# Kernel tuning notes

Hardware: AMD Instinct MI355X
Metric: run time of the kernel (lower is better)

The kernel has to match this reference:

```python
import jax, jax.numpy as jnp
import numpy as np

B = 16384
D_VIS, D_LANG, D_STATE = 768, 768, 64
D = 256          # d_model
E = 4            # n_experts
K = 2            # top_k
D_IN = D_VIS + D_LANG + D_STATE
EPS = 1e-5


def layernorm(x, g, b):
    mu = x.mean(-1, keepdims=True)
    var = ((x - mu) ** 2).mean(-1, keepdims=True)
    return g * (x - mu) / jnp.sqrt(var + EPS) + b


def setup_inputs() -> dict:
    key = jax.random.key(0)
    ks = jax.random.split(key, 16)
    s = 0.02
    return {
        "vis": jax.random.normal(ks[0], (B, D_VIS), jnp.float32),
        "lang": jax.random.normal(ks[1], (B, D_LANG), jnp.float32),
        "state": jax.random.normal(ks[2], (B, D_STATE), jnp.float32),
        # fusion: Linear(d_in, d_model) + LayerNorm
        "Wf": jax.random.normal(ks[3], (D_IN, D), jnp.float32) * s,
        "bf": jnp.zeros((D,), jnp.float32),
        "gf": jnp.ones((D,), jnp.float32),
        "bfln": jnp.zeros((D,), jnp.float32),
        # gate (bias=False); random instead of zeros so routing is nontrivial
        "Wg": jax.random.normal(ks[4], (D, E), jnp.float32) * s,
        # stacked experts: Linear(d,2d) -> GELU -> Linear(2d,d) -> GELU -> Linear(d,d), then LN(x + net(x))
        "W1": jax.random.normal(ks[5], (E, D, 2 * D), jnp.float32) * s,
        "b1": jnp.zeros((E, 2 * D), jnp.float32),
        "W2": jax.random.normal(ks[6], (E, 2 * D, D), jnp.float32) * s,
        "b2": jnp.zeros((E, D), jnp.float32),
        "W3": jax.random.normal(ks[7], (E, D, D), jnp.float32) * s,
        "b3": jnp.zeros((E, D), jnp.float32),
        "eg": jnp.ones((E, D), jnp.float32),
        "eb": jnp.zeros((E, D), jnp.float32),
    }


def reference(vis, lang, state, Wf, bf, gf, bfln, Wg, W1, b1, W2, b2, W3, b3, eg, eb):
    gelu = lambda t: jax.nn.gelu(t, approximate=False)
    # fusion: Linear -> LayerNorm -> GELU  (dropout is eval-mode identity)
    x = jnp.concatenate([vis, lang, state], axis=-1) @ Wf + bf   # [B, D]
    x = gelu(layernorm(x, gf, bfln))

    logits = x @ Wg                                              # [B, E]
    all_probs = jax.nn.softmax(logits, axis=-1)
    top_vals, top_idx = jax.lax.top_k(logits, K)                 # [B, K]
    top_w = jax.nn.softmax(top_vals, axis=-1)                    # [B, K]

    # all experts densely (E small); original computes same math per masked subset
    h = gelu(jnp.einsum('bd,edh->beh', x, W1) + b1)              # [B, E, 2D]
    h = gelu(jnp.einsum('beh,ehd->bed', h, W2) + b2)             # [B, E, D]
    h = jnp.einsum('bed,edf->bef', h, W3) + b3                   # [B, E, D]
    y = layernorm(x[:, None, :] + h, eg, eb)                     # [B, E, D]

    # gather selected experts and combine with top-k weights
    y_sel = jnp.take_along_axis(y, top_idx[:, :, None], axis=1)  # [B, K, D]
    out = jnp.einsum('bk,bkd->bd', top_w, y_sel)                 # [B, D]

    # load-balance loss: importance x load
    counts = jnp.zeros((E,), x.dtype).at[top_idx.reshape(-1)].add(1.0)
    f_i = counts / (B * K)
    lb_loss = E * jnp.sum(f_i * all_probs.mean(0))
    return out, lb_loss
```

## Files before the change

### kernel.cpp

```cpp
#include <hip/hip_runtime.h>
#include <math.h>


typedef unsigned short u16;
typedef unsigned int u32;
typedef __attribute__((ext_vector_type(8))) short bf16x8;
typedef __attribute__((ext_vector_type(4))) float f32x4;

__device__ __forceinline__ float bf2f(u16 u) {
    union { u32 i; float f; } v; v.i = ((u32)u) << 16; return v.f;
}
__device__ __forceinline__ u16 f2bf(float f) {
    union { float f; u32 i; } v; v.f = f;
    u32 x = v.i;
    return (u16)((x + 0x7fffu + ((x >> 16) & 1u)) >> 16);
}
__device__ __forceinline__ float gelu_exact(float v) {
    return 0.5f * v * (1.0f + erff(v * 0.70710678118654752f));
}

typedef __attribute__((address_space(1))) void GV;
typedef __attribute__((address_space(3))) void SV;
__device__ __forceinline__ void gldlds(const void* g, void* l) {
    __builtin_amdgcn_global_load_lds((GV*)g, (SV*)l, 16, 0, 0);
}

__device__ __forceinline__ u32 pk2(u32 f0, u32 f1) {
    return __builtin_amdgcn_perm(f1, f0, 0x07060302);
}

__device__ __forceinline__ void stageA64(const u16* Ag, int lda, u16* As, int tid) {
#pragma unroll
    for (int i = 0; i < 2; ++i) {
        int s = i * 256 + tid;
        int m = s >> 3, c = s & 7;
        gldlds(Ag + m * lda + (c ^ (m & 7)) * 8, As + s * 8);
    }
}
__device__ __forceinline__ void stageA64_R32(const u16* Ag, int lda, u16* As, int tid) {
    int s = tid;
    int m = s >> 3, c = s & 7;
    gldlds(Ag + m * lda + (c ^ (m & 7)) * 8, As + s * 8);
}
__device__ __forceinline__ void stageB64(const u16* Bg, int ldb, u16* Bs, int tid) {
#pragma unroll
    for (int i = 0; i < 8; ++i) {
        int s = i * 256 + tid;
        int n = s >> 3, c = s & 7;
        gldlds(Bg + n * ldb + (c ^ (n & 7)) * 8, Bs + s * 8);
    }
}
__device__ __forceinline__ void compute64(const u16* As, const u16* Bs, f32x4 acc[4][4],
                                          int w, int l16, int quad) {
#pragma unroll
    for (int ks = 0; ks < 2; ++ks) {
        bf16x8 a[4];
#pragma unroll
        for (int mt = 0; mt < 4; ++mt) {
            int m = mt * 16 + l16;
            a[mt] = *(const bf16x8*)(As + m * 64 + (((ks * 4 + quad) ^ (m & 7)) << 3));
        }
#pragma unroll
        for (int nt = 0; nt < 4; ++nt) {
            int n = w * 64 + nt * 16 + l16;
            bf16x8 b = *(const bf16x8*)(Bs + n * 64 + (((ks * 4 + quad) ^ (n & 7)) << 3));
#pragma unroll
            for (int mt = 0; mt < 4; ++mt)
                acc[mt][nt] = __builtin_amdgcn_mfma_f32_16x16x32_bf16(a[mt], b, acc[mt][nt], 0, 0, 0);
        }
    }
}
__device__ __forceinline__ void compute64_R32(const u16* As, const u16* Bs, f32x4 acc[2][4],
                                              int w, int l16, int quad) {
#pragma unroll
    for (int ks = 0; ks < 2; ++ks) {
        bf16x8 a[2];
#pragma unroll
        for (int mt = 0; mt < 2; ++mt) {
            int m = mt * 16 + l16;
            a[mt] = *(const bf16x8*)(As + m * 64 + (((ks * 4 + quad) ^ (m & 7)) << 3));
        }
#pragma unroll
        for (int nt = 0; nt < 4; ++nt) {
            int n = w * 64 + nt * 16 + l16;
            bf16x8 b = *(const bf16x8*)(Bs + n * 64 + (((ks * 4 + quad) ^ (n & 7)) << 3));
#pragma unroll
            for (int mt = 0; mt < 2; ++mt)
                acc[mt][nt] = __builtin_amdgcn_mfma_f32_16x16x32_bf16(a[mt], b, acc[mt][nt], 0, 0, 0);
        }
    }
}

#define SEG_WF  409600
#define SEG_W1  524288
#define SEG_W2  524288
#define SEG_W3  262144
#define PREP_ITEMS (SEG_WF + SEG_W1 + SEG_W2 + SEG_W3 + 8)

__global__ __launch_bounds__(256) void prep_kernel(
    const float* __restrict__ Wf, const float* __restrict__ W1, const float* __restrict__ W2,
    const float* __restrict__ W3,
    u16* __restrict__ wft, u16* __restrict__ w1t, u16* __restrict__ w2t, u16* __restrict__ w3t,
    float* __restrict__ lbacc) {
    int idx = blockIdx.x * 256 + threadIdx.x;
    if (idx < SEG_WF) {
        int n = idx / 1600, k = idx % 1600;
        wft[idx] = f2bf(Wf[(size_t)k * 256 + n]);
        return;
    }
    idx -= SEG_WF;
    if (idx < SEG_W1) {
        int e = idx >> 17, r = idx & 131071;
        int n = r >> 8, k = r & 255;
        w1t[idx] = f2bf(W1[(size_t)e * 131072 + (size_t)k * 512 + n]);
        return;
    }
    idx -= SEG_W1;
    if (idx < SEG_W2) {
        int e = idx >> 17, r = idx & 131071;
        int n = r >> 9, k = r & 511;
        w2t[idx] = f2bf(W2[(size_t)e * 131072 + (size_t)k * 256 + n]);
        return;
    }
    idx -= SEG_W2;
    if (idx < SEG_W3) {
        int e = idx >> 16, r = idx & 65535;
        int n = r >> 8, k = r & 255;
        w3t[idx] = f2bf(W3[(size_t)e * 65536 + (size_t)k * 256 + n]);
        return;
    }
    idx -= SEG_W3;
    if (idx < 8) lbacc[idx] = 0.0f;
}

__global__ __launch_bounds__(256) void fusion_kernel(
    const float* __restrict__ vis, const float* __restrict__ lang, const float* __restrict__ state,
    const u16* __restrict__ BT, const float* __restrict__ bfv_, const float* __restrict__ gf,
    const float* __restrict__ bfln, const float* __restrict__ Wg,
    u16* __restrict__ xbf, float* __restrict__ wr, float* __restrict__ lbacc) {
    __shared__ __align__(16) u32 Af[2048];
    __shared__ __align__(16) u16 Bs[16384];
    int tid = threadIdx.x;
    int w = tid >> 6, lane = tid & 63, quad = lane >> 4, l16 = lane & 15;
    int m0 = blockIdx.x * 32;
    f32x4 acc[2][4] = {};

    for (int kit = 0; kit < 25; ++kit) {
        const float* base; int ld;
        if (kit < 12)      { base = vis   + (size_t)m0 * 768 + kit * 64;        ld = 768; }
        else if (kit < 24) { base = lang  + (size_t)m0 * 768 + (kit - 12) * 64; ld = 768; }
        else               { base = state + (size_t)m0 * 64;                    ld = 64; }
#pragma unroll
        for (int i = 0; i < 2; ++i) {
            int s = i * 256 + tid;
            int m = s >> 4, c = s & 15;
            gldlds(base + m * ld + (c ^ (m & 15)) * 4, Af + s * 4);
        }
        stageB64(BT + kit * 64, 1600, Bs, tid);
        __syncthreads();
#pragma unroll
        for (int ks = 0; ks < 2; ++ks) {
            bf16x8 a[2];
#pragma unroll
            for (int mt = 0; mt < 2; ++mt) {
                int m = mt * 16 + l16;
                int c0 = ks * 8 + quad * 2;
                const u32* rowp = Af + m * 64;
                uint4 f0 = *(const uint4*)(rowp + (c0 ^ (m & 15)) * 4);
                uint4 f1 = *(const uint4*)(rowp + ((c0 + 1) ^ (m & 15)) * 4);
                union { u32 u[4]; bf16x8 v; } pk;
                pk.u[0] = pk2(f0.x, f0.y); pk.u[1] = pk2(f0.z, f0.w);
                pk.u[2] = pk2(f1.x, f1.y); pk.u[3] = pk2(f1.z, f1.w);
                a[mt] = pk.v;
            }
#pragma unroll
            for (int nt = 0; nt < 4; ++nt) {
                int n = w * 64 + nt * 16 + l16;
                bf16x8 b = *(const bf16x8*)(Bs + n * 64 + (((ks * 4 + quad) ^ (n & 7)) << 3));
#pragma unroll
                for (int mt = 0; mt < 2; ++mt)
                    acc[mt][nt] = __builtin_amdgcn_mfma_f32_16x16x32_bf16(a[mt], b, acc[mt][nt], 0, 0, 0);
            }
        }
        __syncthreads();
    }

    float2* red  = (float2*)Af;
    float*  muv  = (float*)(Af + 256);
    float*  rsv  = (float*)(Af + 288);
    float*  gred = (float*)(Af + 512);
    float*  sacc = (float*)(Af + 1024);

    float bv[4], gvv[4], blv[4]; float4 wgv[4];
#pragma unroll
    for (int nt = 0; nt < 4; ++nt) {
        int col = w * 64 + nt * 16 + l16;
        bv[nt] = bfv_[col]; gvv[nt] = gf[col]; blv[nt] = bfln[col];
        wgv[nt] = *(const float4*)(Wg + col * 4);
    }
    if (tid < 8) sacc[tid] = 0.f;
#pragma unroll
    for (int mt = 0; mt < 2; ++mt)
#pragma unroll
        for (int r = 0; r < 4; ++r) {
            float ss = 0.f, qq = 0.f;
#pragma unroll
            for (int nt = 0; nt < 4; ++nt) {
                float v = acc[mt][nt][r] + bv[nt];
                acc[mt][nt][r] = v;
                ss += v; qq += v * v;
            }
#pragma unroll
            for (int d = 1; d < 16; d <<= 1) { ss += __shfl_xor(ss, d); qq += __shfl_xor(qq, d); }
            if (l16 == 0) red[w * 32 + mt * 16 + quad * 4 + r] = make_float2(ss, qq);
        }
    __syncthreads();
    if (tid < 32) {
        float ss = 0.f, qq = 0.f;
#pragma unroll
        for (int ww = 0; ww < 4; ++ww) { float2 t = red[ww * 32 + tid]; ss += t.x; qq += t.y; }
        float mu = ss * (1.f / 256.f);
        float var = qq * (1.f / 256.f) - mu * mu;
        muv[tid] = mu;
        rsv[tid] = 1.f / sqrtf(var + 1e-5f);
    }
    __syncthreads();
#pragma unroll
    for (int mt = 0; mt < 2; ++mt)
#pragma unroll
        for (int r = 0; r < 4; ++r) {
            int rl = mt * 16 + quad * 4 + r;
            float mu = muv[rl], rs = rsv[rl];
#pragma unroll
            for (int nt = 0; nt < 4; ++nt) {
                int col = w * 64 + nt * 16 + l16;
                float t = (acc[mt][nt][r] - mu) * rs * gvv[nt] + blv[nt];
                float g = gelu_exact(t);
                acc[mt][nt][r] = g;
                xbf[(size_t)(m0 + rl) * 256 + col] = f2bf(g);
            }
        }
#pragma unroll
    for (int mt = 0; mt < 2; ++mt)
#pragma unroll
        for (int r = 0; r < 4; ++r) {
            int rl = mt * 16 + quad * 4 + r;
            float p0 = 0.f, p1 = 0.f, p2 = 0.f, p3 = 0.f;
#pragma unroll
            for (int nt = 0; nt < 4; ++nt) {
                float g = acc[mt][nt][r];
                p0 += g * wgv[nt].x; p1 += g * wgv[nt].y;
                p2 += g * wgv[nt].z; p3 += g * wgv[nt].w;
            }
#pragma unroll
            for (int d = 1; d < 16; d <<= 1) {
                p0 += __shfl_xor(p0, d); p1 += __shfl_xor(p1, d);
                p2 += __shfl_xor(p2, d); p3 += __shfl_xor(p3, d);
            }
            if (l16 == 0) {
                float* gp = gred + w * 128 + rl * 4;
                gp[0] = p0; gp[1] = p1; gp[2] = p2; gp[3] = p3;
            }
        }
    __syncthreads();
    if (tid < 32) {
        int row = tid;
        float lg[4];
#pragma unroll
        for (int e = 0; e < 4; ++e)
            lg[e] = gred[row * 4 + e] + gred[128 + row * 4 + e] +
                    gred[256 + row * 4 + e] + gred[384 + row * 4 + e];
        float mx = fmaxf(fmaxf(lg[0], lg[1]), fmaxf(lg[2], lg[3]));
        float ex[4]; float Z = 0.f;
#pragma unroll
        for (int e = 0; e < 4; ++e) { ex[e] = expf(lg[e] - mx); Z += ex[e]; }
        int i0 = 0; float v0 = lg[0];
#pragma unroll
        for (int e = 1; e < 4; ++e) if (lg[e] > v0) { v0 = lg[e]; i0 = e; }
        int i1 = -1; float v1 = -1e30f;
#pragma unroll
        for (int e = 0; e < 4; ++e) if (e != i0 && lg[e] > v1) { v1 = lg[e]; i1 = e; }
        float t = expf(v1 - v0);
        float wA = 1.f / (1.f + t), wB = t / (1.f + t);
        float w4[4] = {0.f, 0.f, 0.f, 0.f};
        w4[i0] = wA; w4[i1] = wB;
#pragma unroll
        for (int e = 0; e < 4; ++e) wr[(size_t)(m0 + row) * 4 + e] = w4[e];
#pragma unroll
        for (int e = 0; e < 4; ++e) atomicAdd(&sacc[e], ex[e] / Z);
        atomicAdd(&sacc[4 + i0], 1.f);
        atomicAdd(&sacc[4 + i1], 1.f);
    }
    __syncthreads();
    if (tid < 8) atomicAdd(lbacc + tid, sacc[tid]);
}

__global__ __launch_bounds__(256) void expert_gemm_kernel(
    const u16* __restrict__ A, int lda, size_t aE,
    const u16* __restrict__ BT, size_t bE,
    const float* __restrict__ bias, int biasE,
    u16* __restrict__ outp, int ldo, size_t oE) {
    __shared__ __align__(16) u16 As[4096];
    __shared__ __align__(16) u16 Bs[16384];
    int tid = threadIdx.x;
    int w = tid >> 6, lane = tid & 63, quad = lane >> 4, l16 = lane & 15;
    int m0 = blockIdx.x * 64;
    int col0 = blockIdx.y * 256;
    int e = blockIdx.z;
    f32x4 acc[4][4] = {};
    const u16* Ag = A + e * aE + (size_t)m0 * lda;
    const u16* Bg = BT + e * bE + (size_t)col0 * lda;
    int kiters = lda >> 6;
    for (int kit = 0; kit < kiters; ++kit) {
        stageA64(Ag + kit * 64, lda, As, tid);
        stageB64(Bg + kit * 64, lda, Bs, tid);
        __syncthreads();
        compute64(As, Bs, acc, w, l16, quad);
        __syncthreads();
    }
#pragma unroll
    for (int nt = 0; nt < 4; ++nt) {
        int col = col0 + w * 64 + nt * 16 + l16;
        float bvv = bias[e * biasE + col];
#pragma unroll
        for (int mt = 0; mt < 4; ++mt)
#pragma unroll
            for (int r = 0; r < 4; ++r) {
                int row = m0 + mt * 16 + quad * 4 + r;
                outp[e * oE + (size_t)row * ldo + col] = f2bf(gelu_exact(acc[mt][nt][r] + bvv));
            }
    }
}

__global__ __launch_bounds__(256) void combine_kernel(
    const u16* __restrict__ h2, const u16* __restrict__ W3T,
    const float* __restrict__ b3, const float* __restrict__ eg, const float* __restrict__ eb,
    const u16* __restrict__ xbf, const float* __restrict__ wr,
    const float* __restrict__ lbacc, float* __restrict__ outp) {
    __shared__ __align__(16) u16 As[2048];
    __shared__ __align__(16) u16 Bs[16384];
    __shared__ __align__(16) u16 xs[8192];
    __shared__ float wl[128];
    int tid = threadIdx.x;
    int w = tid >> 6, lane = tid & 63, quad = lane >> 4, l16 = lane & 15;
    int m0 = blockIdx.x * 32;
    if (blockIdx.x == 0 && tid == 0) {
        float lb = 0.f;
#pragma unroll
        for (int e = 0; e < 4; ++e)
            lb += (lbacc[4 + e] / 32768.f) * (lbacc[e] / 16384.f);
        outp[4194304] = 4.f * lb;
    }
#pragma unroll
    for (int i = 0; i < 4; ++i) {
        int s = i * 256 + tid;
        *(uint4*)(xs + s * 8) = *(const uint4*)(xbf + (size_t)m0 * 256 + s * 8);
    }
    if (tid < 128) wl[tid] = wr[(size_t)m0 * 4 + tid];
    float2* red = (float2*)As;
    float* muv = (float*)((char*)As + 1024);
    float* rsv = (float*)((char*)As + 1152);
    f32x4 oacc[2][4] = {};
    for (int e = 0; e < 4; ++e) {
        __syncthreads();
        f32x4 acc[2][4] = {};
        const u16* Ag = h2 + ((size_t)e * 16384 + m0) * 256;
        const u16* Bg = W3T + (size_t)e * 65536;
        for (int kit = 0; kit < 4; ++kit) {
            stageA64_R32(Ag + kit * 64, 256, As, tid);
            stageB64(Bg + kit * 64, 256, Bs, tid);
            __syncthreads();
            compute64_R32(As, Bs, acc, w, l16, quad);
            __syncthreads();
        }
        float b3v[4], egv[4], ebv[4];
#pragma unroll
        for (int nt = 0; nt < 4; ++nt) {
            int col = w * 64 + nt * 16 + l16;
            b3v[nt] = b3[e * 256 + col]; egv[nt] = eg[e * 256 + col]; ebv[nt] = eb[e * 256 + col];
        }
#pragma unroll
        for (int mt = 0; mt < 2; ++mt)
#pragma unroll
            for (int r = 0; r < 4; ++r) {
                int rl = mt * 16 + quad * 4 + r;
                float ss = 0.f, qq = 0.f;
#pragma unroll
                for (int nt = 0; nt < 4; ++nt) {
                    int col = w * 64 + nt * 16 + l16;
                    float v = acc[mt][nt][r] + b3v[nt] + bf2f(xs[rl * 256 + col]);
                    acc[mt][nt][r] = v;
                    ss += v; qq += v * v;
                }
#pragma unroll
                for (int d = 1; d < 16; d <<= 1) { ss += __shfl_xor(ss, d); qq += __shfl_xor(qq, d); }
                if (l16 == 0) red[w * 32 + rl] = make_float2(ss, qq);
            }
        __syncthreads();
        if (tid < 32) {
            float ss = 0.f, qq = 0.f;
#pragma unroll
            for (int ww = 0; ww < 4; ++ww) { float2 t = red[ww * 32 + tid]; ss += t.x; qq += t.y; }
            float mu = ss * (1.f / 256.f);
            float var = qq * (1.f / 256.f) - mu * mu;
            muv[tid] = mu;
            rsv[tid] = 1.f / sqrtf(var + 1e-5f);
        }
        __syncthreads();
#pragma unroll
        for (int mt = 0; mt < 2; ++mt)
#pragma unroll
            for (int r = 0; r < 4; ++r) {
                int rl = mt * 16 + quad * 4 + r;
                float mu = muv[rl], rs = rsv[rl], we = wl[rl * 4 + e];
#pragma unroll
                for (int nt = 0; nt < 4; ++nt) {
                    float y = (acc[mt][nt][r] - mu) * rs * egv[nt] + ebv[nt];
                    oacc[mt][nt][r] += we * y;
                }
            }
    }
#pragma unroll
    for (int mt = 0; mt < 2; ++mt)
#pragma unroll
        for (int r = 0; r < 4; ++r) {
            int rl = mt * 16 + quad * 4 + r;
#pragma unroll
            for (int nt = 0; nt < 4; ++nt) {
                int col = w * 64 + nt * 16 + l16;
                outp[(size_t)(m0 + rl) * 256 + col] = oacc[mt][nt][r];
            }
        }
}

extern "C" void kernel_launch(void* const* d_in, const int* in_sizes, int n_in,
                              void* d_out, int out_size, void* d_ws, size_t ws_size,
                              hipStream_t stream) {
    const float* vis   = (const float*)d_in[0];
    const float* lang  = (const float*)d_in[1];
    const float* state = (const float*)d_in[2];
    const float* Wf    = (const float*)d_in[3];
    const float* bf_   = (const float*)d_in[4];
    const float* gf    = (const float*)d_in[5];
    const float* bfln  = (const float*)d_in[6];
    const float* Wg    = (const float*)d_in[7];
    const float* W1    = (const float*)d_in[8];
    const float* b1    = (const float*)d_in[9];
    const float* W2    = (const float*)d_in[10];
    const float* b2    = (const float*)d_in[11];
    const float* W3    = (const float*)d_in[12];
    const float* b3    = (const float*)d_in[13];
    const float* eg    = (const float*)d_in[14];
    const float* eb    = (const float*)d_in[15];
    float* outp = (float*)d_out;

    char* ws = (char*)d_ws;
    size_t off = 0;
    float* lbacc = (float*)(ws + off); off += 256;
    u16* WFT  = (u16*)(ws + off); off += 819200UL;
    u16* W1T  = (u16*)(ws + off); off += 1048576UL;
    u16* W2T  = (u16*)(ws + off); off += 1048576UL;
    u16* W3T  = (u16*)(ws + off); off += 524288UL;
    u16* XBF  = (u16*)(ws + off); off += 8388608UL;
    float* WR = (float*)(ws + off); off += 262144UL;
    u16* H1   = (u16*)(ws + off); off += 67108864UL;
    u16* H2   = (u16*)(ws + off); off += 33554432UL;
    if (ws_size < off) return;

    int prep_blocks = (PREP_ITEMS + 255) / 256;
    prep_kernel<<<prep_blocks, 256, 0, stream>>>(Wf, W1, W2, W3, WFT, W1T, W2T, W3T, lbacc);
    fusion_kernel<<<512, 256, 0, stream>>>(vis, lang, state, WFT, bf_, gf, bfln, Wg,
                                           XBF, WR, lbacc);
    expert_gemm_kernel<<<dim3(256, 2, 4), 256, 0, stream>>>(
        XBF, 256, 0, W1T, 131072, b1, 512, H1, 512, 8388608UL);
    expert_gemm_kernel<<<dim3(256, 1, 4), 256, 0, stream>>>(
        H1, 512, 8388608UL, W2T, 131072, b2, 256, H2, 256, 4194304UL);
    combine_kernel<<<512, 256, 0, stream>>>(H2, W3T, b3, eg, eb, XBF, WR, lbacc, outp);
}
```

Before: 324.5 us.

## Double-buffer LDS staging in fusion, expert and combine GEMM kernels

Turns the GEMM loops in all three kernels into double-buffered pipelines. The next K-tile is loaded asynchronously via global_load_lds while the current one is computed, using explicit vmcnt waits and raw barriers in place of __syncthreads. The combine kernel also flattens its expert and K loops into one 16-step pipeline, and moves the residual x tile into registers so it can reuse LDS. This is meant to hide global load latency. The cost is doubled LDS, which may reduce occupancy, and the hand-counted vmcnt values must match the number of issued loads.

```diff
diff --git a/kernel.cpp b/kernel.cpp
--- a/kernel.cpp
+++ b/kernel.cpp
@@ -28,6 +28,20 @@
 __device__ __forceinline__ u32 pk2(u32 f0, u32 f1) {
     return __builtin_amdgcn_perm(f1, f0, 0x07060302);
 }
+
+#define WAIT_VM(N) asm volatile("s_waitcnt vmcnt(" #N ")" ::: "memory")
+#define BARRIER()                                    \
+    do {                                             \
+        asm volatile("" ::: "memory");               \
+        __builtin_amdgcn_s_barrier();                \
+        asm volatile("" ::: "memory");               \
+    } while (0)
+#define LGKBAR()                                            \
+    do {                                                    \
+        asm volatile("s_waitcnt lgkmcnt(0)" ::: "memory");  \
+        __builtin_amdgcn_s_barrier();                       \
+        asm volatile("" ::: "memory");                      \
+    } while (0)
 
 __device__ __forceinline__ void stageA64(const u16* Ag, int lda, u16* As, int tid) {
 #pragma unroll
@@ -138,14 +152,14 @@
     const u16* __restrict__ BT, const float* __restrict__ bfv_, const float* __restrict__ gf,
     const float* __restrict__ bfln, const float* __restrict__ Wg,
     u16* __restrict__ xbf, float* __restrict__ wr, float* __restrict__ lbacc) {
-    __shared__ __align__(16) u32 Af[2048];
-    __shared__ __align__(16) u16 Bs[16384];
+    __shared__ __align__(16) u32 Af[2][2048];
+    __shared__ __align__(16) u16 Bs[2][16384];
     int tid = threadIdx.x;
     int w = tid >> 6, lane = tid & 63, quad = lane >> 4, l16 = lane & 15;
     int m0 = blockIdx.x * 32;
     f32x4 acc[2][4] = {};
 
-    for (int kit = 0; kit < 25; ++kit) {
+    auto stage = [&](int b, int kit) {
         const float* base; int ld;
         if (kit < 12)      { base = vis   + (size_t)m0 * 768 + kit * 64;        ld = 768; }
         else if (kit < 24) { base = lang  + (size_t)m0 * 768 + (kit - 12) * 64; ld = 768; }
@@ -154,10 +168,17 @@
         for (int i = 0; i < 2; ++i) {
             int s = i * 256 + tid;
             int m = s >> 4, c = s & 15;
-            gldlds(base + m * ld + (c ^ (m & 15)) * 4, Af + s * 4);
-        }
-        stageB64(BT + kit * 64, 1600, Bs, tid);
-        __syncthreads();
+            gldlds(base + m * ld + (c ^ (m & 15)) * 4, &Af[b][s * 4]);
+        }
+        stageB64(BT + kit * 64, 1600, Bs[b], tid);
+    };
+
+    stage(0, 0);
+    for (int kit = 0; kit < 25; ++kit) {
+        int cur = kit & 1;
+        if (kit + 1 < 25) { stage(cur ^ 1, kit + 1); WAIT_VM(10); }
+        else              { WAIT_VM(0); }
+        BARRIER();
 #pragma unroll
         for (int ks = 0; ks < 2; ++ks) {
             bf16x8 a[2];
@@ -165,7 +186,7 @@
             for (int mt = 0; mt < 2; ++mt) {
                 int m = mt * 16 + l16;
                 int c0 = ks * 8 + quad * 2;
-                const u32* rowp = Af + m * 64;
+                const u32* rowp = &Af[cur][m * 64];
                 uint4 f0 = *(const uint4*)(rowp + (c0 ^ (m & 15)) * 4);
                 uint4 f1 = *(const uint4*)(rowp + ((c0 + 1) ^ (m & 15)) * 4);
                 union { u32 u[4]; bf16x8 v; } pk;
@@ -176,20 +197,21 @@
 #pragma unroll
             for (int nt = 0; nt < 4; ++nt) {
                 int n = w * 64 + nt * 16 + l16;
-                bf16x8 b = *(const bf16x8*)(Bs + n * 64 + (((ks * 4 + quad) ^ (n & 7)) << 3));
+                bf16x8 b = *(const bf16x8*)(Bs[cur] + n * 64 + (((ks * 4 + quad) ^ (n & 7)) << 3));
 #pragma unroll
                 for (int mt = 0; mt < 2; ++mt)
                     acc[mt][nt] = __builtin_amdgcn_mfma_f32_16x16x32_bf16(a[mt], b, acc[mt][nt], 0, 0, 0);
             }
         }
-        __syncthreads();
-    }
-
-    float2* red  = (float2*)Af;
-    float*  muv  = (float*)(Af + 256);
-    float*  rsv  = (float*)(Af + 288);
-    float*  gred = (float*)(Af + 512);
-    float*  sacc = (float*)(Af + 1024);
+        BARRIER();
+    }
+
+    u32* Af0 = &Af[0][0];
+    float2* red  = (float2*)Af0;
+    float*  muv  = (float*)(Af0 + 256);
+    float*  rsv  = (float*)(Af0 + 288);
+    float*  gred = (float*)(Af0 + 512);
+    float*  sacc = (float*)(Af0 + 1024);
 
     float bv[4], gvv[4], blv[4]; float4 wgv[4];
 #pragma unroll
@@ -300,8 +322,8 @@
     const u16* __restrict__ BT, size_t bE,
     const float* __restrict__ bias, int biasE,
     u16* __restrict__ outp, int ldo, size_t oE) {
-    __shared__ __align__(16) u16 As[4096];
-    __shared__ __align__(16) u16 Bs[16384];
+    __shared__ __align__(16) u16 As[2][4096];
+    __shared__ __align__(16) u16 Bs[2][16384];
     int tid = threadIdx.x;
     int w = tid >> 6, lane = tid & 63, quad = lane >> 4, l16 = lane & 15;
     int m0 = blockIdx.x * 64;
@@ -311,12 +333,18 @@
     const u16* Ag = A + e * aE + (size_t)m0 * lda;
     const u16* Bg = BT + e * bE + (size_t)col0 * lda;
     int kiters = lda >> 6;
+    stageA64(Ag, lda, As[0], tid);
+    stageB64(Bg, lda, Bs[0], tid);
     for (int kit = 0; kit < kiters; ++kit) {
-        stageA64(Ag + kit * 64, lda, As, tid);
-        stageB64(Bg + kit * 64, lda, Bs, tid);
-        __syncthreads();
-        compute64(As, Bs, acc, w, l16, quad);
-        __syncthreads();
+        int cur = kit & 1;
+        if (kit + 1 < kiters) {
+            stageA64(Ag + (kit + 1) * 64, lda, As[cur ^ 1], tid);
+            stageB64(Bg + (kit + 1) * 64, lda, Bs[cur ^ 1], tid);
+            WAIT_VM(10);
+        } else { WAIT_VM(0); }
+        BARRIER();
+        compute64(As[cur], Bs[cur], acc, w, l16, quad);
+        BARRIER();
     }
 #pragma unroll
     for (int nt = 0; nt < 4; ++nt) {
@@ -337,10 +365,11 @@
     const float* __restrict__ b3, const float* __restrict__ eg, const float* __restrict__ eb,
     const u16* __restrict__ xbf, const float* __restrict__ wr,
     const float* __restrict__ lbacc, float* __restrict__ outp) {
-    __shared__ __align__(16) u16 As[2048];
-    __shared__ __align__(16) u16 Bs[16384];
-    __shared__ __align__(16) u16 xs[8192];
+    __shared__ __align__(16) u16 As[2][2048];
+    __shared__ __align__(16) u16 Bs[2][16384];
     __shared__ float wl[128];
+    __shared__ float2 red[128];
+    __shared__ float muv[32], rsv[32];
     int tid = threadIdx.x;
     int w = tid >> 6, lane = tid & 63, quad = lane >> 4, l16 = lane & 15;
     int m0 = blockIdx.x * 32;
@@ -351,74 +380,92 @@
             lb += (lbacc[4 + e] / 32768.f) * (lbacc[e] / 16384.f);
         outp[4194304] = 4.f * lb;
     }
+    u16* xs = &Bs[0][0];
 #pragma unroll
     for (int i = 0; i < 4; ++i) {
         int s = i * 256 + tid;
         *(uint4*)(xs + s * 8) = *(const uint4*)(xbf + (size_t)m0 * 256 + s * 8);
     }
     if (tid < 128) wl[tid] = wr[(size_t)m0 * 4 + tid];
-    float2* red = (float2*)As;
-    float* muv = (float*)((char*)As + 1024);
-    float* rsv = (float*)((char*)As + 1152);
+    __syncthreads();
+    float xr[2][4][4];
+#pragma unroll
+    for (int mt = 0; mt < 2; ++mt)
+#pragma unroll
+        for (int r = 0; r < 4; ++r) {
+            int rl = mt * 16 + quad * 4 + r;
+#pragma unroll
+            for (int nt = 0; nt < 4; ++nt) {
+                int col = w * 64 + nt * 16 + l16;
+                xr[mt][r][nt] = bf2f(xs[rl * 256 + col]);
+            }
+        }
+    __syncthreads();
+
     f32x4 oacc[2][4] = {};
-    for (int e = 0; e < 4; ++e) {
-        __syncthreads();
-        f32x4 acc[2][4] = {};
-        const u16* Ag = h2 + ((size_t)e * 16384 + m0) * 256;
-        const u16* Bg = W3T + (size_t)e * 65536;
-        for (int kit = 0; kit < 4; ++kit) {
-            stageA64_R32(Ag + kit * 64, 256, As, tid);
-            stageB64(Bg + kit * 64, 256, Bs, tid);
-            __syncthreads();
-            compute64_R32(As, Bs, acc, w, l16, quad);
-            __syncthreads();
-        }
-        float b3v[4], egv[4], ebv[4];
-#pragma unroll
-        for (int nt = 0; nt < 4; ++nt) {
-            int col = w * 64 + nt * 16 + l16;
-            b3v[nt] = b3[e * 256 + col]; egv[nt] = eg[e * 256 + col]; ebv[nt] = eb[e * 256 + col];
-        }
-#pragma unroll
-        for (int mt = 0; mt < 2; ++mt)
-#pragma unroll
-            for (int r = 0; r < 4; ++r) {
-                int rl = mt * 16 + quad * 4 + r;
+    f32x4 acc[2][4] = {};
+    auto stage = [&](int b, int p) {
+        int ee = p >> 2, kit = p & 3;
+        stageA64_R32(h2 + ((size_t)ee * 16384 + m0) * 256 + kit * 64, 256, As[b], tid);
+        stageB64(W3T + (size_t)ee * 65536 + kit * 64, 256, Bs[b], tid);
+    };
+    stage(0, 0);
+    for (int p = 0; p < 16; ++p) {
+        int cur = p & 1;
+        if (p + 1 < 16) { stage(cur ^ 1, p + 1); WAIT_VM(9); }
+        else            { WAIT_VM(0); }
+        BARRIER();
+        compute64_R32(As[cur], Bs[cur], acc, w, l16, quad);
+        BARRIER();
+        if ((p & 3) == 3) {
+            int e = p >> 2;
+            float b3v[4], egv[4], ebv[4];
+#pragma unroll
+            for (int nt = 0; nt < 4; ++nt) {
+                int col = w * 64 + nt * 16 + l16;
+                b3v[nt] = b3[e * 256 + col]; egv[nt] = eg[e * 256 + col]; ebv[nt] = eb[e * 256 + col];
+            }
+#pragma unroll
+            for (int mt = 0; mt < 2; ++mt)
+#pragma unroll
+                for (int r = 0; r < 4; ++r) {
+                    int rl = mt * 16 + quad * 4 + r;
+                    float ss = 0.f, qq = 0.f;
+#pragma unroll
+                    for (int nt = 0; nt < 4; ++nt) {
+                        float v = acc[mt][nt][r] + b3v[nt] + xr[mt][r][nt];
+                        acc[mt][nt][r] = v;
+                        ss += v; qq += v * v;
+                    }
+#pragma unroll
+                    for (int d = 1; d < 16; d <<= 1) { ss += __shfl_xor(ss, d); qq += __shfl_xor(qq, d); }
+                    if (l16 == 0) red[w * 32 + rl] = make_float2(ss, qq);
+                }
+            LGKBAR();
+            if (tid < 32) {
                 float ss = 0.f, qq = 0.f;
 #pragma unroll
-                for (int nt = 0; nt < 4; ++nt) {
-                    int col = w * 64 + nt * 16 + l16;
-                    float v = acc[mt][nt][r] + b3v[nt] + bf2f(xs[rl * 256 + col]);
-                    acc[mt][nt][r] = v;
-                    ss += v; qq += v * v;
+                for (int ww = 0; ww < 4; ++ww) { float2 t = red[ww * 32 + tid]; ss += t.x; qq += t.y; }
+                float mu = ss * (1.f / 256.f);
+                float var = qq * (1.f / 256.f) - mu * mu;
+                muv[tid] = mu;
+                rsv[tid] = 1.f / sqrtf(var + 1e-5f);
+            }
+            LGKBAR();
+#pragma unroll
+            for (int mt = 0; mt < 2; ++mt)
+#pragma unroll
+                for (int r = 0; r < 4; ++r) {
+                    int rl = mt * 16 + quad * 4 + r;
+                    float mu = muv[rl], rs = rsv[rl], we = wl[rl * 4 + e];
+#pragma unroll
+                    for (int nt = 0; nt < 4; ++nt) {
+                        float y = (acc[mt][nt][r] - mu) * rs * egv[nt] + ebv[nt];
+                        oacc[mt][nt][r] += we * y;
+                        acc[mt][nt][r] = 0.f;
+                    }
                 }
-#pragma unroll
-                for (int d = 1; d < 16; d <<= 1) { ss += __shfl_xor(ss, d); qq += __shfl_xor(qq, d); }
-                if (l16 == 0) red[w * 32 + rl] = make_float2(ss, qq);
-            }
-        __syncthreads();
-        if (tid < 32) {
-            float ss = 0.f, qq = 0.f;
-#pragma unroll
-            for (int ww = 0; ww < 4; ++ww) { float2 t = red[ww * 32 + tid]; ss += t.x; qq += t.y; }
-            float mu = ss * (1.f / 256.f);
-            float var = qq * (1.f / 256.f) - mu * mu;
-            muv[tid] = mu;
-            rsv[tid] = 1.f / sqrtf(var + 1e-5f);
-        }
-        __syncthreads();
-#pragma unroll
-        for (int mt = 0; mt < 2; ++mt)
-#pragma unroll
-            for (int r = 0; r < 4; ++r) {
-                int rl = mt * 16 + quad * 4 + r;
-                float mu = muv[rl], rs = rsv[rl], we = wl[rl * 4 + e];
-#pragma unroll
-                for (int nt = 0; nt < 4; ++nt) {
-                    float y = (acc[mt][nt][r] - mu) * rs * egv[nt] + ebv[nt];
-                    oacc[mt][nt][r] += we * y;
-                }
-            }
+        }
     }
 #pragma unroll
     for (int mt = 0; mt < 2; ++mt)
```

Measured after the change: 355.8 us. 1.1x slower.

## Double-buffer LDS staging in fusion, expert GEMM and combine kernels

Applied to the files above, without the earlier changes.

Adds ping-pong LDS buffers to all three GEMM kernels so the loads for the next K-slice are issued before computing the current one, leaving one barrier per step. The combine kernel now also runs a single 16-step pipeline across experts and K, calls the LN epilogue every four steps, and holds the residual x in registers instead of a separate LDS array. This is meant to hide global-load latency behind MFMA work. In exchange LDS use roughly doubles, which can lower occupancy, and register pressure rises from the cached residual.

```diff
diff --git a/kernel.cpp b/kernel.cpp
--- a/kernel.cpp
+++ b/kernel.cpp
@@ -138,14 +138,16 @@
     const u16* __restrict__ BT, const float* __restrict__ bfv_, const float* __restrict__ gf,
     const float* __restrict__ bfln, const float* __restrict__ Wg,
     u16* __restrict__ xbf, float* __restrict__ wr, float* __restrict__ lbacc) {
-    __shared__ __align__(16) u32 Af[2048];
-    __shared__ __align__(16) u16 Bs[16384];
+    __shared__ __align__(16) u32 AfA[2048];
+    __shared__ __align__(16) u32 AfB[2048];
+    __shared__ __align__(16) u16 BsA[16384];
+    __shared__ __align__(16) u16 BsB[16384];
     int tid = threadIdx.x;
     int w = tid >> 6, lane = tid & 63, quad = lane >> 4, l16 = lane & 15;
     int m0 = blockIdx.x * 32;
     f32x4 acc[2][4] = {};
 
-    for (int kit = 0; kit < 25; ++kit) {
+    auto stageK = [&](u32* Af, u16* Bs, int kit) {
         const float* base; int ld;
         if (kit < 12)      { base = vis   + (size_t)m0 * 768 + kit * 64;        ld = 768; }
         else if (kit < 24) { base = lang  + (size_t)m0 * 768 + (kit - 12) * 64; ld = 768; }
@@ -157,7 +159,8 @@
             gldlds(base + m * ld + (c ^ (m & 15)) * 4, Af + s * 4);
         }
         stageB64(BT + kit * 64, 1600, Bs, tid);
-        __syncthreads();
+    };
+    auto computeK = [&](const u32* Af, const u16* Bs) {
 #pragma unroll
         for (int ks = 0; ks < 2; ++ks) {
             bf16x8 a[2];
@@ -182,14 +185,27 @@
                     acc[mt][nt] = __builtin_amdgcn_mfma_f32_16x16x32_bf16(a[mt], b, acc[mt][nt], 0, 0, 0);
             }
         }
-        __syncthreads();
-    }
-
-    float2* red  = (float2*)Af;
-    float*  muv  = (float*)(Af + 256);
-    float*  rsv  = (float*)(Af + 288);
-    float*  gred = (float*)(Af + 512);
-    float*  sacc = (float*)(Af + 1024);
+    };
+
+    stageK(AfA, BsA, 0);
+    __syncthreads();
+    for (int kit = 0; kit < 24; kit += 2) {
+        stageK(AfB, BsB, kit + 1);
+        computeK(AfA, BsA);
+        __syncthreads();
+        if (kit + 2 < 25) stageK(AfA, BsA, kit + 2);
+        computeK(AfB, BsB);
+        __syncthreads();
+    }
+    computeK(AfA, BsA);
+    __syncthreads();
+
+    u32* Af0 = AfA;
+    float2* red  = (float2*)Af0;
+    float*  muv  = (float*)(Af0 + 256);
+    float*  rsv  = (float*)(Af0 + 288);
+    float*  gred = (float*)(Af0 + 512);
+    float*  sacc = (float*)(Af0 + 1024);
 
     float bv[4], gvv[4], blv[4]; float4 wgv[4];
 #pragma unroll
@@ -300,8 +316,10 @@
     const u16* __restrict__ BT, size_t bE,
     const float* __restrict__ bias, int biasE,
     u16* __restrict__ outp, int ldo, size_t oE) {
-    __shared__ __align__(16) u16 As[4096];
-    __shared__ __align__(16) u16 Bs[16384];
+    __shared__ __align__(16) u16 AsA[4096];
+    __shared__ __align__(16) u16 AsB[4096];
+    __shared__ __align__(16) u16 BsA[16384];
+    __shared__ __align__(16) u16 BsB[16384];
     int tid = threadIdx.x;
     int w = tid >> 6, lane = tid & 63, quad = lane >> 4, l16 = lane & 15;
     int m0 = blockIdx.x * 64;
@@ -311,11 +329,19 @@
     const u16* Ag = A + e * aE + (size_t)m0 * lda;
     const u16* Bg = BT + e * bE + (size_t)col0 * lda;
     int kiters = lda >> 6;
-    for (int kit = 0; kit < kiters; ++kit) {
-        stageA64(Ag + kit * 64, lda, As, tid);
-        stageB64(Bg + kit * 64, lda, Bs, tid);
-        __syncthreads();
-        compute64(As, Bs, acc, w, l16, quad);
+    stageA64(Ag, lda, AsA, tid);
+    stageB64(Bg, lda, BsA, tid);
+    __syncthreads();
+    for (int kit = 0; kit < kiters; kit += 2) {
+        stageA64(Ag + (kit + 1) * 64, lda, AsB, tid);
+        stageB64(Bg + (kit + 1) * 64, lda, BsB, tid);
+        compute64(AsA, BsA, acc, w, l16, quad);
+        __syncthreads();
+        if (kit + 2 < kiters) {
+            stageA64(Ag + (kit + 2) * 64, lda, AsA, tid);
+            stageB64(Bg + (kit + 2) * 64, lda, BsA, tid);
+        }
+        compute64(AsB, BsB, acc, w, l16, quad);
         __syncthreads();
     }
 #pragma unroll
@@ -337,10 +363,13 @@
     const float* __restrict__ b3, const float* __restrict__ eg, const float* __restrict__ eb,
     const u16* __restrict__ xbf, const float* __restrict__ wr,
     const float* __restrict__ lbacc, float* __restrict__ outp) {
-    __shared__ __align__(16) u16 As[2048];
-    __shared__ __align__(16) u16 Bs[16384];
-    __shared__ __align__(16) u16 xs[8192];
+    __shared__ __align__(16) u16 AsA[2048];
+    __shared__ __align__(16) u16 AsB[2048];
+    __shared__ __align__(16) u16 BsA[16384];
+    __shared__ __align__(16) u16 BsB[16384];
     __shared__ float wl[128];
+    __shared__ float2 red[128];
+    __shared__ float muv[32], rsv[32];
     int tid = threadIdx.x;
     int w = tid >> 6, lane = tid & 63, quad = lane >> 4, l16 = lane & 15;
     int m0 = blockIdx.x * 32;
@@ -351,28 +380,36 @@
             lb += (lbacc[4 + e] / 32768.f) * (lbacc[e] / 16384.f);
         outp[4194304] = 4.f * lb;
     }
+    u16* xs = BsA;
 #pragma unroll
     for (int i = 0; i < 4; ++i) {
         int s = i * 256 + tid;
         *(uint4*)(xs + s * 8) = *(const uint4*)(xbf + (size_t)m0 * 256 + s * 8);
     }
     if (tid < 128) wl[tid] = wr[(size_t)m0 * 4 + tid];
-    float2* red = (float2*)As;
-    float* muv = (float*)((char*)As + 1024);
-    float* rsv = (float*)((char*)As + 1152);
+    __syncthreads();
+    float xr[2][4][4];
+#pragma unroll
+    for (int mt = 0; mt < 2; ++mt)
+#pragma unroll
+        for (int r = 0; r < 4; ++r) {
+            int rl = mt * 16 + quad * 4 + r;
+#pragma unroll
+            for (int nt = 0; nt < 4; ++nt) {
+                int col = w * 64 + nt * 16 + l16;
+                xr[mt][r][nt] = bf2f(xs[rl * 256 + col]);
+            }
+        }
+    __syncthreads();
+
     f32x4 oacc[2][4] = {};
-    for (int e = 0; e < 4; ++e) {
-        __syncthreads();
-        f32x4 acc[2][4] = {};
-        const u16* Ag = h2 + ((size_t)e * 16384 + m0) * 256;
-        const u16* Bg = W3T + (size_t)e * 65536;
-        for (int kit = 0; kit < 4; ++kit) {
-            stageA64_R32(Ag + kit * 64, 256, As, tid);
-            stageB64(Bg + kit * 64, 256, Bs, tid);
-            __syncthreads();
-            compute64_R32(As, Bs, acc, w, l16, quad);
-            __syncthreads();
-        }
+    f32x4 acc[2][4] = {};
+    auto stageP = [&](u16* As, u16* Bs, int p) {
+        int ee = p >> 2, kit = p & 3;
+        stageA64_R32(h2 + ((size_t)ee * 16384 + m0) * 256 + kit * 64, 256, As, tid);
+        stageB64(W3T + (size_t)ee * 65536 + kit * 64, 256, Bs, tid);
+    };
+    auto epilogue = [&](int e) {
         float b3v[4], egv[4], ebv[4];
 #pragma unroll
         for (int nt = 0; nt < 4; ++nt) {
@@ -387,8 +424,7 @@
                 float ss = 0.f, qq = 0.f;
 #pragma unroll
                 for (int nt = 0; nt < 4; ++nt) {
-                    int col = w * 64 + nt * 16 + l16;
-                    float v = acc[mt][nt][r] + b3v[nt] + bf2f(xs[rl * 256 + col]);
+                    float v = acc[mt][nt][r] + b3v[nt] + xr[mt][r][nt];
                     acc[mt][nt][r] = v;
                     ss += v; qq += v * v;
                 }
@@ -417,8 +453,21 @@
                 for (int nt = 0; nt < 4; ++nt) {
                     float y = (acc[mt][nt][r] - mu) * rs * egv[nt] + ebv[nt];
                     oacc[mt][nt][r] += we * y;
+                    acc[mt][nt][r] = 0.f;
                 }
             }
+    };
+
+    stageP(AsA, BsA, 0);
+    __syncthreads();
+    for (int p = 0; p < 16; p += 2) {
+        stageP(AsB, BsB, p + 1);
+        compute64_R32(AsA, BsA, acc, w, l16, quad);
+        __syncthreads();
+        if (p + 2 < 16) stageP(AsA, BsA, p + 2);
+        compute64_R32(AsB, BsB, acc, w, l16, quad);
+        __syncthreads();
+        if ((p & 3) == 2) epilogue(p >> 2);
     }
 #pragma unroll
     for (int mt = 0; mt < 2; ++mt)
```

New measurement: 343.1 us. 5.7% more time.

## Use 512-thread blocks in fusion and combine kernels, splitting N across 8 waves

Applied to the files above, without the earlier changes.

Doubles threads per block for the fusion and combine kernels, so each of 8 waves computes a 32-column slice instead of 64 columns. Staging loops, reductions and LayerNorm partial sums are rewritten for 8 waves. In combine, the residual x tile is read once into registers via the B buffer, which frees the separate shared buffer. The aim is more waves in flight to hide memory latency with a grid of only 512 blocks. In exchange there is more synchronisation and cross-wave reduction, and each wave issues fewer MFMAs per shared B load.

```diff
diff --git a/kernel.cpp b/kernel.cpp
--- a/kernel.cpp
+++ b/kernel.cpp
@@ -37,11 +37,6 @@
         gldlds(Ag + m * lda + (c ^ (m & 7)) * 8, As + s * 8);
     }
 }
-__device__ __forceinline__ void stageA64_R32(const u16* Ag, int lda, u16* As, int tid) {
-    int s = tid;
-    int m = s >> 3, c = s & 7;
-    gldlds(Ag + m * lda + (c ^ (m & 7)) * 8, As + s * 8);
-}
 __device__ __forceinline__ void stageB64(const u16* Bg, int ldb, u16* Bs, int tid) {
 #pragma unroll
     for (int i = 0; i < 8; ++i) {
@@ -50,6 +45,21 @@
         gldlds(Bg + n * ldb + (c ^ (n & 7)) * 8, Bs + s * 8);
     }
 }
+__device__ __forceinline__ void stageA32_512(const u16* Ag, int lda, u16* As, int tid) {
+    if (tid < 256) {
+        int m = tid >> 3, c = tid & 7;
+        gldlds(Ag + m * lda + (c ^ (m & 7)) * 8, As + tid * 8);
+    }
+}
+__device__ __forceinline__ void stageB64_512(const u16* Bg, int ldb, u16* Bs, int tid) {
+#pragma unroll
+    for (int i = 0; i < 4; ++i) {
+        int s = i * 512 + tid;
+        int n = s >> 3, c = s & 7;
+        gldlds(Bg + n * ldb + (c ^ (n & 7)) * 8, Bs + s * 8);
+    }
+}
+
 __device__ __forceinline__ void compute64(const u16* As, const u16* Bs, f32x4 acc[4][4],
                                           int w, int l16, int quad) {
 #pragma unroll
@@ -70,8 +80,8 @@
         }
     }
 }
-__device__ __forceinline__ void compute64_R32(const u16* As, const u16* Bs, f32x4 acc[2][4],
-                                              int w, int l16, int quad) {
+__device__ __forceinline__ void compute32_8w(const u16* As, const u16* Bs, f32x4 acc[2][2],
+                                             int w, int l16, int quad) {
 #pragma unroll
     for (int ks = 0; ks < 2; ++ks) {
         bf16x8 a[2];
@@ -81,8 +91,8 @@
             a[mt] = *(const bf16x8*)(As + m * 64 + (((ks * 4 + quad) ^ (m & 7)) << 3));
         }
 #pragma unroll
-        for (int nt = 0; nt < 4; ++nt) {
-            int n = w * 64 + nt * 16 + l16;
+        for (int nt = 0; nt < 2; ++nt) {
+            int n = w * 32 + nt * 16 + l16;
             bf16x8 b = *(const bf16x8*)(Bs + n * 64 + (((ks * 4 + quad) ^ (n & 7)) << 3));
 #pragma unroll
             for (int mt = 0; mt < 2; ++mt)
@@ -133,7 +143,7 @@
     if (idx < 8) lbacc[idx] = 0.0f;
 }
 
-__global__ __launch_bounds__(256) void fusion_kernel(
+__global__ __launch_bounds__(512, 4) void fusion_kernel(
     const float* __restrict__ vis, const float* __restrict__ lang, const float* __restrict__ state,
     const u16* __restrict__ BT, const float* __restrict__ bfv_, const float* __restrict__ gf,
     const float* __restrict__ bfln, const float* __restrict__ Wg,
@@ -143,20 +153,19 @@
     int tid = threadIdx.x;
     int w = tid >> 6, lane = tid & 63, quad = lane >> 4, l16 = lane & 15;
     int m0 = blockIdx.x * 32;
-    f32x4 acc[2][4] = {};
+    f32x4 acc[2][2] = {};
 
     for (int kit = 0; kit < 25; ++kit) {
         const float* base; int ld;
         if (kit < 12)      { base = vis   + (size_t)m0 * 768 + kit * 64;        ld = 768; }
         else if (kit < 24) { base = lang  + (size_t)m0 * 768 + (kit - 12) * 64; ld = 768; }
         else               { base = state + (size_t)m0 * 64;                    ld = 64; }
-#pragma unroll
-        for (int i = 0; i < 2; ++i) {
-            int s = i * 256 + tid;
+        {
+            int s = tid;
             int m = s >> 4, c = s & 15;
             gldlds(base + m * ld + (c ^ (m & 15)) * 4, Af + s * 4);
         }
-        stageB64(BT + kit * 64, 1600, Bs, tid);
+        stageB64_512(BT + kit * 64, 1600, Bs, tid);
         __syncthreads();
 #pragma unroll
         for (int ks = 0; ks < 2; ++ks) {
@@ -174,8 +183,8 @@
                 a[mt] = pk.v;
             }
 #pragma unroll
-            for (int nt = 0; nt < 4; ++nt) {
-                int n = w * 64 + nt * 16 + l16;
+            for (int nt = 0; nt < 2; ++nt) {
+                int n = w * 32 + nt * 16 + l16;
                 bf16x8 b = *(const bf16x8*)(Bs + n * 64 + (((ks * 4 + quad) ^ (n & 7)) << 3));
 #pragma unroll
                 for (int mt = 0; mt < 2; ++mt)
@@ -186,15 +195,15 @@
     }
 
     float2* red  = (float2*)Af;
-    float*  muv  = (float*)(Af + 256);
-    float*  rsv  = (float*)(Af + 288);
-    float*  gred = (float*)(Af + 512);
-    float*  sacc = (float*)(Af + 1024);
-
-    float bv[4], gvv[4], blv[4]; float4 wgv[4];
-#pragma unroll
-    for (int nt = 0; nt < 4; ++nt) {
-        int col = w * 64 + nt * 16 + l16;
+    float*  muv  = (float*)(Af + 512);
+    float*  rsv  = (float*)(Af + 544);
+    float*  gred = (float*)(Af + 576);
+    float*  sacc = (float*)(Af + 1600);
+
+    float bv[2], gvv[2], blv[2]; float4 wgv[2];
+#pragma unroll
+    for (int nt = 0; nt < 2; ++nt) {
+        int col = w * 32 + nt * 16 + l16;
         bv[nt] = bfv_[col]; gvv[nt] = gf[col]; blv[nt] = bfln[col];
         wgv[nt] = *(const float4*)(Wg + col * 4);
     }
@@ -205,7 +214,7 @@
         for (int r = 0; r < 4; ++r) {
             float ss = 0.f, qq = 0.f;
 #pragma unroll
-            for (int nt = 0; nt < 4; ++nt) {
+            for (int nt = 0; nt < 2; ++nt) {
                 float v = acc[mt][nt][r] + bv[nt];
                 acc[mt][nt][r] = v;
                 ss += v; qq += v * v;
@@ -218,7 +227,7 @@
     if (tid < 32) {
         float ss = 0.f, qq = 0.f;
 #pragma unroll
-        for (int ww = 0; ww < 4; ++ww) { float2 t = red[ww * 32 + tid]; ss += t.x; qq += t.y; }
+        for (int ww = 0; ww < 8; ++ww) { float2 t = red[ww * 32 + tid]; ss += t.x; qq += t.y; }
         float mu = ss * (1.f / 256.f);
         float var = qq * (1.f / 256.f) - mu * mu;
         muv[tid] = mu;
@@ -232,8 +241,8 @@
             int rl = mt * 16 + quad * 4 + r;
             float mu = muv[rl], rs = rsv[rl];
 #pragma unroll
-            for (int nt = 0; nt < 4; ++nt) {
-                int col = w * 64 + nt * 16 + l16;
+            for (int nt = 0; nt < 2; ++nt) {
+                int col = w * 32 + nt * 16 + l16;
                 float t = (acc[mt][nt][r] - mu) * rs * gvv[nt] + blv[nt];
                 float g = gelu_exact(t);
                 acc[mt][nt][r] = g;
@@ -247,7 +256,7 @@
             int rl = mt * 16 + quad * 4 + r;
             float p0 = 0.f, p1 = 0.f, p2 = 0.f, p3 = 0.f;
 #pragma unroll
-            for (int nt = 0; nt < 4; ++nt) {
+            for (int nt = 0; nt < 2; ++nt) {
                 float g = acc[mt][nt][r];
                 p0 += g * wgv[nt].x; p1 += g * wgv[nt].y;
                 p2 += g * wgv[nt].z; p3 += g * wgv[nt].w;
@@ -267,9 +276,12 @@
         int row = tid;
         float lg[4];
 #pragma unroll
-        for (int e = 0; e < 4; ++e)
-            lg[e] = gred[row * 4 + e] + gred[128 + row * 4 + e] +
-                    gred[256 + row * 4 + e] + gred[384 + row * 4 + e];
+        for (int e = 0; e < 4; ++e) {
+            float s = 0.f;
+#pragma unroll
+            for (int ww = 0; ww < 8; ++ww) s += gred[ww * 128 + row * 4 + e];
+            lg[e] = s;
+        }
         float mx = fmaxf(fmaxf(lg[0], lg[1]), fmaxf(lg[2], lg[3]));
         float ex[4]; float Z = 0.f;
 #pragma unroll
@@ -332,15 +344,16 @@
     }
 }
 
-__global__ __launch_bounds__(256) void combine_kernel(
+__global__ __launch_bounds__(512, 4) void combine_kernel(
     const u16* __restrict__ h2, const u16* __restrict__ W3T,
     const float* __restrict__ b3, const float* __restrict__ eg, const float* __restrict__ eb,
     const u16* __restrict__ xbf, const float* __restrict__ wr,
     const float* __restrict__ lbacc, float* __restrict__ outp) {
     __shared__ __align__(16) u16 As[2048];
     __shared__ __align__(16) u16 Bs[16384];
-    __shared__ __align__(16) u16 xs[8192];
     __shared__ float wl[128];
+    __shared__ float2 red[256];
+    __shared__ float muv[32], rsv[32];
     int tid = threadIdx.x;
     int w = tid >> 6, lane = tid & 63, quad = lane >> 4, l16 = lane & 15;
     int m0 = blockIdx.x * 32;
@@ -352,31 +365,42 @@
         outp[4194304] = 4.f * lb;
     }
 #pragma unroll
-    for (int i = 0; i < 4; ++i) {
-        int s = i * 256 + tid;
-        *(uint4*)(xs + s * 8) = *(const uint4*)(xbf + (size_t)m0 * 256 + s * 8);
+    for (int i = 0; i < 2; ++i) {
+        int s = i * 512 + tid;
+        *(uint4*)(Bs + s * 8) = *(const uint4*)(xbf + (size_t)m0 * 256 + s * 8);
     }
     if (tid < 128) wl[tid] = wr[(size_t)m0 * 4 + tid];
-    float2* red = (float2*)As;
-    float* muv = (float*)((char*)As + 1024);
-    float* rsv = (float*)((char*)As + 1152);
-    f32x4 oacc[2][4] = {};
+    __syncthreads();
+    float xr[2][4][2];
+#pragma unroll
+    for (int mt = 0; mt < 2; ++mt)
+#pragma unroll
+        for (int r = 0; r < 4; ++r) {
+            int rl = mt * 16 + quad * 4 + r;
+#pragma unroll
+            for (int nt = 0; nt < 2; ++nt) {
+                int col = w * 32 + nt * 16 + l16;
+                xr[mt][r][nt] = bf2f(Bs[rl * 256 + col]);
+            }
+        }
+    __syncthreads();
+
+    f32x4 oacc[2][2] = {};
     for (int e = 0; e < 4; ++e) {
-        __syncthreads();
-        f32x4 acc[2][4] = {};
+        f32x4 acc[2][2] = {};
         const u16* Ag = h2 + ((size_t)e * 16384 + m0) * 256;
         const u16* Bg = W3T + (size_t)e * 65536;
         for (int kit = 0; kit < 4; ++kit) {
-            stageA64_R32(Ag + kit * 64, 256, As, tid);
-            stageB64(Bg + kit * 64, 256, Bs, tid);
+            stageA32_512(Ag + kit * 64, 256, As, tid);
+            stageB64_512(Bg + kit * 64, 256, Bs, tid);
             __syncthreads();
-            compute64_R32(As, Bs, acc, w, l16, quad);
+            compute32_8w(As, Bs, acc, w, l16, quad);
             __syncthreads();
         }
-        float b3v[4], egv[4], ebv[4];
-#pragma unroll
-        for (int nt = 0; nt < 4; ++nt) {
-            int col = w * 64 + nt * 16 + l16;
+        float b3v[2], egv[2], ebv[2];
+#pragma unroll
+        for (int nt = 0; nt < 2; ++nt) {
+            int col = w * 32 + nt * 16 + l16;
             b3v[nt] = b3[e * 256 + col]; egv[nt] = eg[e * 256 + col]; ebv[nt] = eb[e * 256 + col];
         }
 #pragma unroll
@@ -386,9 +410,8 @@
                 int rl = mt * 16 + quad * 4 + r;
                 float ss = 0.f, qq = 0.f;
 #pragma unroll
-                for (int nt = 0; nt < 4; ++nt) {
-                    int col = w * 64 + nt * 16 + l16;
-                    float v = acc[mt][nt][r] + b3v[nt] + bf2f(xs[rl * 256 + col]);
+                for (int nt = 0; nt < 2; ++nt) {
+                    float v = acc[mt][nt][r] + b3v[nt] + xr[mt][r][nt];
                     acc[mt][nt][r] = v;
                     ss += v; qq += v * v;
                 }
@@ -400,7 +423,7 @@
         if (tid < 32) {
             float ss = 0.f, qq = 0.f;
 #pragma unroll
-            for (int ww = 0; ww < 4; ++ww) { float2 t = red[ww * 32 + tid]; ss += t.x; qq += t.y; }
+            for (int ww = 0; ww < 8; ++ww) { float2 t = red[ww * 32 + tid]; ss += t.x; qq += t.y; }
             float mu = ss * (1.f / 256.f);
             float var = qq * (1.f / 256.f) - mu * mu;
             muv[tid] = mu;
@@ -414,7 +437,7 @@
                 int rl = mt * 16 + quad * 4 + r;
                 float mu = muv[rl], rs = rsv[rl], we = wl[rl * 4 + e];
 #pragma unroll
-                for (int nt = 0; nt < 4; ++nt) {
+                for (int nt = 0; nt < 2; ++nt) {
                     float y = (acc[mt][nt][r] - mu) * rs * egv[nt] + ebv[nt];
                     oacc[mt][nt][r] += we * y;
                 }
@@ -426,8 +449,8 @@
         for (int r = 0; r < 4; ++r) {
             int rl = mt * 16 + quad * 4 + r;
 #pragma unroll
-            for (int nt = 0; nt < 4; ++nt) {
-                int col = w * 64 + nt * 16 + l16;
+            for (int nt = 0; nt < 2; ++nt) {
+                int col = w * 32 + nt * 16 + l16;
                 outp[(size_t)(m0 + rl) * 256 + col] = oacc[mt][nt][r];
             }
         }
@@ -469,11 +492,11 @@
 
     int prep_blocks = (PREP_ITEMS + 255) / 256;
     prep_kernel<<<prep_blocks, 256, 0, stream>>>(Wf, W1, W2, W3, WFT, W1T, W2T, W3T, lbacc);
-    fusion_kernel<<<512, 256, 0, stream>>>(vis, lang, state, WFT, bf_, gf, bfln, Wg,
+    fusion_kernel<<<512, 512, 0, stream>>>(vis, lang, state, WFT, bf_, gf, bfln, Wg,
                                            XBF, WR, lbacc);
     expert_gemm_kernel<<<dim3(256, 2, 4), 256, 0, stream>>>(
         XBF, 256, 0, W1T, 131072, b1, 512, H1, 512, 8388608UL);
     expert_gemm_kernel<<<dim3(256, 1, 4), 256, 0, stream>>>(
         H1, 512, 8388608UL, W2T, 131072, b2, 256, H2, 256, 4194304UL);
-    combine_kernel<<<512, 256, 0, stream>>>(H2, W3T, b3, eg, eb, XBF, WR, lbacc, outp);
-}
+    combine_kernel<<<512, 512, 0, stream>>>(H2, W3T, b3, eg, eb, XBF, WR, lbacc, outp);
+}
```

Result: slower. 338.3 us (+4.3%).
